# Performance work log

Hardware: AMD Instinct MI355X
Metric: run time of the kernel (lower is better)

Reference implementation:

```python
import jax, jax.numpy as jnp
import numpy as np

V = 512          # num vertices
F = 64           # pair-feature dim (gpnn_channels in)
C = 64           # gpnn_channels out
E = 8192         # num edges (avg degree 16)


def setup_inputs() -> dict:
    key = jax.random.key(0)
    k1, k2, k3, k4 = jax.random.split(key, 4)
    alpha = jax.random.normal(k1, (V * V, F), dtype=jnp.float32)          # pair features, row v*V+w
    edge_index = jax.random.randint(k2, (2, E), 0, V)                      # COO [src; dst]
    # GPNNEdgeConv.nn = MLP([F, C, C], act='relu')  (norm treated as identity / eval stats)
    w1 = jax.random.normal(k3, (F, C), dtype=jnp.float32) * (1.0 / np.sqrt(F))
    b1 = jnp.zeros((C,), dtype=jnp.float32)
    w2 = jax.random.normal(k4, (C, C), dtype=jnp.float32) * (1.0 / np.sqrt(C))
    b2 = jnp.zeros((C,), dtype=jnp.float32)
    eps = jnp.asarray(0.0, dtype=jnp.float32)                              # train_eps parameter
    return {"alpha": alpha, "edge_index": edge_index,
            "w1": w1, "b1": b1, "w2": w2, "b2": b2, "eps": eps}


def reference(alpha, edge_index, w1, b1, w2, b2, eps):
    # Dense 0/1 adjacency adj_t: adj[v, j] = 1 iff edge j -> v (dst-indexed, as spmm(adj_t, .)).
    adj = jnp.zeros((V, V), dtype=alpha.dtype).at[edge_index[1], edge_index[0]].set(1.0)
    a3 = alpha.reshape(V, V, F)  # a3[v, j] = alpha[v*V + j]
    # message_and_aggregate: out[v*V+w] = row v of spmm(adj_t, A_{v,w}),
    # where A_{v,w}[j] = alpha[v*V+j] + alpha[w*V+j]  (sum aggregation)
    #   = sum_j adj[v,j] * (a3[v,j] + a3[w,j]) = S[v] + T[v,w]
    S = jnp.einsum('vj,vjf->vf', adj, a3)    # [V, F]
    T = jnp.einsum('vj,wjf->vwf', adj, a3)   # [V, V, F]
    out = (S[:, None, :] + T).reshape(V * V, F)
    # GINConv residual: out + (1 + eps) * x_r, then MLP (Linear-ReLU-Linear)
    out = out + (1.0 + eps) * alpha
    h = jax.nn.relu(out @ w1 + b1)
    return h @ w2 + b2
```

## Files before the change

### kernel.cpp

```cpp
#include <hip/hip_runtime.h>
#include <hip/hip_bf16.h>

#define NV 512
#define NF 64
#define SCR_STRIDE 72
#define MASK_STRIDE 17

typedef __attribute__((ext_vector_type(8))) short bf16x8;
typedef __attribute__((ext_vector_type(4))) float f32x4;

union BF8 { bf16x8 v; unsigned u[4]; };

__device__ __forceinline__ unsigned short f2bf(float x) {
    unsigned u = __float_as_uint(x);
    unsigned r = (u + 0x7fffu + ((u >> 16) & 1u)) >> 16;
    return (unsigned short)r;
}

__global__ void k_zero(unsigned int* mask) {
    mask[blockIdx.x * 256 + threadIdx.x] = 0u;
}

__global__ void k_edges(const int* __restrict__ ei, int E, unsigned int* __restrict__ mask) {
    int e = blockIdx.x * 256 + threadIdx.x;
    if (e < E) {
        int s = ei[e];
        int d = ei[E + e];
        atomicOr(&mask[d * 16 + (s >> 5)], 1u << (s & 31));
    }
}

__global__ void k_S(const unsigned int* __restrict__ mask, const float* __restrict__ alpha,
                    float* __restrict__ S) {
    int v = blockIdx.x;
    int f = threadIdx.x;
    float acc = 0.f;
    for (int wd = 0; wd < 16; ++wd) {
        unsigned int bits = mask[v * 16 + wd];
        while (bits) {
            int b = __ffs(bits) - 1;
            bits &= bits - 1;
            int j = wd * 32 + b;
            acc += alpha[((size_t)v * NV + j) * NF + f];
        }
    }
    S[v * NF + f] = acc;
}

#define AWT_OFF  0
#define MASK_OFF 65536
#define SCR_OFF  100352

__global__ __launch_bounds__(512, 1) void k_main(
    const float* __restrict__ alpha, const float* __restrict__ w1, const float* __restrict__ b1,
    const float* __restrict__ w2, const float* __restrict__ b2, const float* __restrict__ eps_p,
    const unsigned int* __restrict__ mask, const float* __restrict__ S,
    float* __restrict__ out)
{
    extern __shared__ char smem[];
    unsigned int* maskL = (unsigned int*)(smem + MASK_OFF);
    unsigned short* scr = (unsigned short*)(smem + SCR_OFF);

    const int w    = blockIdx.x;
    const int t    = threadIdx.x;
    const int lane = t & 63;
    const int wid  = t >> 6;
    const int nlo  = lane & 15;
    const int g    = lane >> 4;
    const int kbase = g * 8;
    const float ceps = 1.0f + eps_p[0];

    bf16x8 w1f[2][4], w2f[2][4];
#pragma unroll
    for (int ks = 0; ks < 2; ++ks)
#pragma unroll
        for (int nt = 0; nt < 4; ++nt) {
            bf16x8 a, b;
#pragma unroll
            for (int e = 0; e < 8; ++e) {
                int k = ks * 32 + kbase + e;
                a[e] = (short)f2bf(w1[k * NF + nt * 16 + nlo]);
                b[e] = (short)f2bf(w2[k * NF + nt * 16 + nlo]);
            }
            w1f[ks][nt] = a;
            w2f[ks][nt] = b;
        }
    float b1v[4], b2v[4];
#pragma unroll
    for (int nt = 0; nt < 4; ++nt) {
        b1v[nt] = b1[nt * 16 + nlo];
        b2v[nt] = b2[nt * 16 + nlo];
    }

    {
        const float* src = alpha + (size_t)w * (NV * NF);
#pragma unroll
        for (int i = 0; i < 2; ++i) {
            int task = i * 512 + t;
            int jb = task >> 4;
            int fq = task & 15;
            f32x4 rows[8];
#pragma unroll
            for (int r = 0; r < 8; ++r)
                rows[r] = *(const f32x4*)(src + (size_t)(jb * 8 + r) * NF + fq * 4);
#pragma unroll
            for (int c = 0; c < 4; ++c) {
                int f = fq * 4 + c;
                BF8 p;
#pragma unroll
                for (int h = 0; h < 4; ++h) {
                    unsigned lo = f2bf(rows[2 * h][c]);
                    unsigned hi = f2bf(rows[2 * h + 1][c]);
                    p.u[h] = lo | (hi << 16);
                }
                int byte = f * 1024 + jb * 16;
                *(bf16x8*)(smem + (byte ^ ((f & 7) << 4))) = p.v;
            }
        }
#pragma unroll
        for (int q = 0; q < 16; ++q) {
            int idx = q * 512 + t;
            maskL[(idx >> 4) * MASK_STRIDE + (idx & 15)] = mask[idx];
        }
    }
    __syncthreads();

    const int mbase = wid * 64;
    f32x4 acc[4][4];
#pragma unroll
    for (int mi = 0; mi < 4; ++mi)
#pragma unroll
        for (int nt = 0; nt < 4; ++nt)
            acc[mi][nt] = (f32x4){0.f, 0.f, 0.f, 0.f};

    const unsigned swz = (unsigned)((nlo & 7) << 4);
    for (int kk = 0; kk < 16; ++kk) {
        bf16x8 bfr[4];
#pragma unroll
        for (int nt = 0; nt < 4; ++nt) {
            int f = nt * 16 + nlo;
            unsigned byte = (unsigned)(f * 1024 + kk * 64 + g * 16);
            bfr[nt] = *(const bf16x8*)(smem + (byte ^ swz));
        }
#pragma unroll
        for (int mi = 0; mi < 4; ++mi) {
            unsigned word = maskL[(mbase + mi * 16 + nlo) * MASK_STRIDE + kk];
            unsigned byteb = (word >> (g * 8)) & 0xFFu;
            BF8 a;
#pragma unroll
            for (int h = 0; h < 4; ++h) {
                unsigned b0 = (byteb >> (2 * h)) & 1u;
                unsigned b1 = (byteb >> (2 * h + 1)) & 1u;
                a.u[h] = (b0 ? 0x3F80u : 0u) | (b1 ? 0x3F800000u : 0u);
            }
#pragma unroll
            for (int nt = 0; nt < 4; ++nt)
                acc[mi][nt] = __builtin_amdgcn_mfma_f32_16x16x32_bf16(a.v, bfr[nt], acc[mi][nt], 0, 0, 0);
        }
    }

    unsigned short* myscr = scr + wid * 16 * SCR_STRIDE;
#pragma unroll
    for (int mi = 0; mi < 4; ++mi) {
        int v0 = mbase + mi * 16;
#pragma unroll
        for (int nt = 0; nt < 4; ++nt) {
            int f = nt * 16 + nlo;
#pragma unroll
            for (int r = 0; r < 4; ++r) {
                int v = v0 + g * 4 + r;
                float pre = acc[mi][nt][r] + S[v * NF + f]
                          + ceps * alpha[((size_t)v * NV + w) * NF + f];
                myscr[(g * 4 + r) * SCR_STRIDE + f] = f2bf(pre);
            }
        }

        bf16x8 a0 = *(const bf16x8*)(myscr + nlo * SCR_STRIDE + kbase);
        bf16x8 a1 = *(const bf16x8*)(myscr + nlo * SCR_STRIDE + 32 + kbase);
        f32x4 accm[4];
#pragma unroll
        for (int nt = 0; nt < 4; ++nt) {
            f32x4 z = {0.f, 0.f, 0.f, 0.f};
            z = __builtin_amdgcn_mfma_f32_16x16x32_bf16(a0, w1f[0][nt], z, 0, 0, 0);
            z = __builtin_amdgcn_mfma_f32_16x16x32_bf16(a1, w1f[1][nt], z, 0, 0, 0);
            accm[nt] = z;
        }

#pragma unroll
        for (int nt = 0; nt < 4; ++nt)
#pragma unroll
            for (int r = 0; r < 4; ++r) {
                float hv = accm[nt][r] + b1v[nt];
                hv = hv > 0.f ? hv : 0.f;
                myscr[(g * 4 + r) * SCR_STRIDE + nt * 16 + nlo] = f2bf(hv);
            }

        bf16x8 h0 = *(const bf16x8*)(myscr + nlo * SCR_STRIDE + kbase);
        bf16x8 h1 = *(const bf16x8*)(myscr + nlo * SCR_STRIDE + 32 + kbase);
#pragma unroll
        for (int nt = 0; nt < 4; ++nt) {
            f32x4 z = {0.f, 0.f, 0.f, 0.f};
            z = __builtin_amdgcn_mfma_f32_16x16x32_bf16(h0, w2f[0][nt], z, 0, 0, 0);
            z = __builtin_amdgcn_mfma_f32_16x16x32_bf16(h1, w2f[1][nt], z, 0, 0, 0);
#pragma unroll
            for (int r = 0; r < 4; ++r) {
                int vv = v0 + g * 4 + r;
                out[((size_t)vv * NV + w) * NF + nt * 16 + nlo] = z[r] + b2v[nt];
            }
        }
    }
}

extern "C" void kernel_launch(void* const* d_in, const int* in_sizes, int n_in,
                              void* d_out, int out_size, void* d_ws, size_t ws_size,
                              hipStream_t stream) {
    const float* alpha = (const float*)d_in[0];
    const int*   ei    = (const int*)d_in[1];
    const float* w1    = (const float*)d_in[2];
    const float* b1    = (const float*)d_in[3];
    const float* w2    = (const float*)d_in[4];
    const float* b2    = (const float*)d_in[5];
    const float* eps   = (const float*)d_in[6];
    float* out = (float*)d_out;
    int E = in_sizes[1] / 2;

    unsigned int* mask = (unsigned int*)d_ws;
    float* S = (float*)d_ws + 8192;

    k_zero <<<32, 256, 0, stream>>>(mask);
    k_edges<<<(E + 255) / 256, 256, 0, stream>>>(ei, E, mask);
    k_S    <<<NV, 64, 0, stream>>>(mask, alpha, S);

    const int smem_bytes = 118784;
    hipFuncSetAttribute(reinterpret_cast<const void*>(k_main),
                        hipFuncAttributeMaxDynamicSharedMemorySize, smem_bytes);
    k_main <<<NV, 512, smem_bytes, stream>>>(alpha, w1, b1, w2, b2, eps, mask, S, out);
}
```

Measured before the change: 68.26 us.

## Shrink LDS footprint by holding adjacency mask in registers and reshuffling

Drops the LDS copy of the adjacency mask. Each lane now loads its mask words into registers and broadcasts them with cross-lane shuffles during the aggregation GEMM. The per-wave scratch is swizzled at 128-byte rows instead of padded, and the alpha-transpose swizzle gains an extra XOR term. Weight fragments are now loaded after the main loop to ease register pressure, and the launch-bounds hint rises from 1 to 4. Together these cut dynamic LDS from 118784 to 81920 bytes to allow more resident blocks per CU, at the cost of extra shuffle instructions and possible register-limit pressure.

```diff
diff --git a/kernel.cpp b/kernel.cpp
--- a/kernel.cpp
+++ b/kernel.cpp
@@ -3,8 +3,6 @@
 
 #define NV 512
 #define NF 64
-#define SCR_STRIDE 72
-#define MASK_STRIDE 17
 
 typedef __attribute__((ext_vector_type(8))) short bf16x8;
 typedef __attribute__((ext_vector_type(4))) float f32x4;
@@ -15,6 +13,10 @@
     unsigned u = __float_as_uint(x);
     unsigned r = (u + 0x7fffu + ((u >> 16) & 1u)) >> 16;
     return (unsigned short)r;
+}
+
+__device__ __forceinline__ unsigned awt_addr(int f, int jbyte) {
+    return (unsigned)((f * 1024 + jbyte) ^ (((f ^ (f >> 3)) & 7) << 4));
 }
 
 __global__ void k_zero(unsigned int* mask) {
@@ -47,19 +49,15 @@
     S[v * NF + f] = acc;
 }
 
-#define AWT_OFF  0
-#define MASK_OFF 65536
-#define SCR_OFF  100352
-
-__global__ __launch_bounds__(512, 1) void k_main(
+#define SCR_OFF 65536
+
+__global__ __launch_bounds__(512, 4) void k_main(
     const float* __restrict__ alpha, const float* __restrict__ w1, const float* __restrict__ b1,
     const float* __restrict__ w2, const float* __restrict__ b2, const float* __restrict__ eps_p,
     const unsigned int* __restrict__ mask, const float* __restrict__ S,
     float* __restrict__ out)
 {
     extern __shared__ char smem[];
-    unsigned int* maskL = (unsigned int*)(smem + MASK_OFF);
-    unsigned short* scr = (unsigned short*)(smem + SCR_OFF);
 
     const int w    = blockIdx.x;
     const int t    = threadIdx.x;
@@ -70,28 +68,6 @@
     const int kbase = g * 8;
     const float ceps = 1.0f + eps_p[0];
 
-    bf16x8 w1f[2][4], w2f[2][4];
-#pragma unroll
-    for (int ks = 0; ks < 2; ++ks)
-#pragma unroll
-        for (int nt = 0; nt < 4; ++nt) {
-            bf16x8 a, b;
-#pragma unroll
-            for (int e = 0; e < 8; ++e) {
-                int k = ks * 32 + kbase + e;
-                a[e] = (short)f2bf(w1[k * NF + nt * 16 + nlo]);
-                b[e] = (short)f2bf(w2[k * NF + nt * 16 + nlo]);
-            }
-            w1f[ks][nt] = a;
-            w2f[ks][nt] = b;
-        }
-    float b1v[4], b2v[4];
-#pragma unroll
-    for (int nt = 0; nt < 4; ++nt) {
-        b1v[nt] = b1[nt * 16 + nlo];
-        b2v[nt] = b2[nt * 16 + nlo];
-    }
-
     {
         const float* src = alpha + (size_t)w * (NV * NF);
 #pragma unroll
@@ -113,19 +89,21 @@
                     unsigned hi = f2bf(rows[2 * h + 1][c]);
                     p.u[h] = lo | (hi << 16);
                 }
-                int byte = f * 1024 + jb * 16;
-                *(bf16x8*)(smem + (byte ^ ((f & 7) << 4))) = p.v;
-            }
-        }
-#pragma unroll
-        for (int q = 0; q < 16; ++q) {
-            int idx = q * 512 + t;
-            maskL[(idx >> 4) * MASK_STRIDE + (idx & 15)] = mask[idx];
-        }
-    }
+                *(bf16x8*)(smem + awt_addr(f, jb * 16)) = p.v;
+            }
+        }
+    }
+
+    const int mbase = wid * 64;
+    unsigned qm[4][4];
+#pragma unroll
+    for (int mi = 0; mi < 4; ++mi) {
+        const uint4 q = *(const uint4*)(mask + (size_t)(mbase + mi * 16 + nlo) * 16 + g * 4);
+        qm[mi][0] = q.x; qm[mi][1] = q.y; qm[mi][2] = q.z; qm[mi][3] = q.w;
+    }
+
     __syncthreads();
 
-    const int mbase = wid * 64;
     f32x4 acc[4][4];
 #pragma unroll
     for (int mi = 0; mi < 4; ++mi)
@@ -133,33 +111,59 @@
         for (int nt = 0; nt < 4; ++nt)
             acc[mi][nt] = (f32x4){0.f, 0.f, 0.f, 0.f};
 
-    const unsigned swz = (unsigned)((nlo & 7) << 4);
-    for (int kk = 0; kk < 16; ++kk) {
-        bf16x8 bfr[4];
-#pragma unroll
-        for (int nt = 0; nt < 4; ++nt) {
-            int f = nt * 16 + nlo;
-            unsigned byte = (unsigned)(f * 1024 + kk * 64 + g * 16);
-            bfr[nt] = *(const bf16x8*)(smem + (byte ^ swz));
-        }
-#pragma unroll
-        for (int mi = 0; mi < 4; ++mi) {
-            unsigned word = maskL[(mbase + mi * 16 + nlo) * MASK_STRIDE + kk];
-            unsigned byteb = (word >> (g * 8)) & 0xFFu;
-            BF8 a;
-#pragma unroll
-            for (int h = 0; h < 4; ++h) {
-                unsigned b0 = (byteb >> (2 * h)) & 1u;
-                unsigned b1 = (byteb >> (2 * h + 1)) & 1u;
-                a.u[h] = (b0 ? 0x3F80u : 0u) | (b1 ? 0x3F800000u : 0u);
-            }
-#pragma unroll
-            for (int nt = 0; nt < 4; ++nt)
-                acc[mi][nt] = __builtin_amdgcn_mfma_f32_16x16x32_bf16(a.v, bfr[nt], acc[mi][nt], 0, 0, 0);
-        }
-    }
-
-    unsigned short* myscr = scr + wid * 16 * SCR_STRIDE;
+#pragma unroll
+    for (int kq = 0; kq < 4; ++kq)
+#pragma unroll
+        for (int kr = 0; kr < 4; ++kr) {
+            const int kk = kq * 4 + kr;
+            bf16x8 bfr[4];
+#pragma unroll
+            for (int nt = 0; nt < 4; ++nt) {
+                int f = nt * 16 + nlo;
+                bfr[nt] = *(const bf16x8*)(smem + awt_addr(f, kk * 64 + g * 16));
+            }
+            const int srcl = kq * 16 + nlo;
+#pragma unroll
+            for (int mi = 0; mi < 4; ++mi) {
+                unsigned word = (unsigned)__shfl((int)qm[mi][kr], srcl);
+                unsigned byteb = (word >> (g * 8)) & 0xFFu;
+                BF8 a;
+#pragma unroll
+                for (int h = 0; h < 4; ++h) {
+                    unsigned b0 = (byteb >> (2 * h)) & 1u;
+                    unsigned b1 = (byteb >> (2 * h + 1)) & 1u;
+                    a.u[h] = (b0 ? 0x3F80u : 0u) | (b1 ? 0x3F800000u : 0u);
+                }
+#pragma unroll
+                for (int nt = 0; nt < 4; ++nt)
+                    acc[mi][nt] = __builtin_amdgcn_mfma_f32_16x16x32_bf16(a.v, bfr[nt], acc[mi][nt], 0, 0, 0);
+            }
+        }
+
+    bf16x8 w1f[2][4], w2f[2][4];
+#pragma unroll
+    for (int ks = 0; ks < 2; ++ks)
+#pragma unroll
+        for (int nt = 0; nt < 4; ++nt) {
+            bf16x8 a, b;
+#pragma unroll
+            for (int e = 0; e < 8; ++e) {
+                int k = ks * 32 + kbase + e;
+                a[e] = (short)f2bf(w1[k * NF + nt * 16 + nlo]);
+                b[e] = (short)f2bf(w2[k * NF + nt * 16 + nlo]);
+            }
+            w1f[ks][nt] = a;
+            w2f[ks][nt] = b;
+        }
+    float b1v[4], b2v[4];
+#pragma unroll
+    for (int nt = 0; nt < 4; ++nt) {
+        b1v[nt] = b1[nt * 16 + nlo];
+        b2v[nt] = b2[nt * 16 + nlo];
+    }
+
+    char* myscr = smem + SCR_OFF + wid * 2048;
+
 #pragma unroll
     for (int mi = 0; mi < 4; ++mi) {
         int v0 = mbase + mi * 16;
@@ -171,12 +175,13 @@
                 int v = v0 + g * 4 + r;
                 float pre = acc[mi][nt][r] + S[v * NF + f]
                           + ceps * alpha[((size_t)v * NV + w) * NF + f];
-                myscr[(g * 4 + r) * SCR_STRIDE + f] = f2bf(pre);
-            }
-        }
-
-        bf16x8 a0 = *(const bf16x8*)(myscr + nlo * SCR_STRIDE + kbase);
-        bf16x8 a1 = *(const bf16x8*)(myscr + nlo * SCR_STRIDE + 32 + kbase);
+                int row = g * 4 + r;
+                *(unsigned short*)(myscr + row * 128 + ((2 * f) ^ ((row & 7) << 4))) = f2bf(pre);
+            }
+        }
+
+        bf16x8 a0 = *(const bf16x8*)(myscr + nlo * 128 + ((g * 16) ^ ((nlo & 7) << 4)));
+        bf16x8 a1 = *(const bf16x8*)(myscr + nlo * 128 + ((g * 16 + 64) ^ ((nlo & 7) << 4)));
         f32x4 accm[4];
 #pragma unroll
         for (int nt = 0; nt < 4; ++nt) {
@@ -192,11 +197,12 @@
             for (int r = 0; r < 4; ++r) {
                 float hv = accm[nt][r] + b1v[nt];
                 hv = hv > 0.f ? hv : 0.f;
-                myscr[(g * 4 + r) * SCR_STRIDE + nt * 16 + nlo] = f2bf(hv);
-            }
-
-        bf16x8 h0 = *(const bf16x8*)(myscr + nlo * SCR_STRIDE + kbase);
-        bf16x8 h1 = *(const bf16x8*)(myscr + nlo * SCR_STRIDE + 32 + kbase);
+                int row = g * 4 + r;
+                *(unsigned short*)(myscr + row * 128 + ((2 * (nt * 16 + nlo)) ^ ((row & 7) << 4))) = f2bf(hv);
+            }
+
+        bf16x8 h0 = *(const bf16x8*)(myscr + nlo * 128 + ((g * 16) ^ ((nlo & 7) << 4)));
+        bf16x8 h1 = *(const bf16x8*)(myscr + nlo * 128 + ((g * 16 + 64) ^ ((nlo & 7) << 4)));
 #pragma unroll
         for (int nt = 0; nt < 4; ++nt) {
             f32x4 z = {0.f, 0.f, 0.f, 0.f};
@@ -231,7 +237,7 @@
     k_edges<<<(E + 255) / 256, 256, 0, stream>>>(ei, E, mask);
     k_S    <<<NV, 64, 0, stream>>>(mask, alpha, S);
 
-    const int smem_bytes = 118784;
+    const int smem_bytes = 81920;
     hipFuncSetAttribute(reinterpret_cast<const void*>(k_main),
                         hipFuncAttributeMaxDynamicSharedMemorySize, smem_bytes);
     k_main <<<NV, 512, smem_bytes, stream>>>(alpha, w1, b1, w2, b2, eps, mask, S, out);
```

Result: slower. 104.9 us (+53.7%).
